# Performance work log

Measured on AMD Instinct MI355X. Metric: run time of the kernel, lower is better.

The kernel has to match this reference:

```python
import jax, jax.numpy as jnp
import numpy as np

KH, KW = 3, 3
PAD = 1
C_IN, C_OUT = 64, 128


def unfold(x, kh, kw, pad):
    # x: (B, C, H, W) -> (B, C, kh*kw, H*W), torch.nn.functional.unfold ordering
    B, C, H, W = x.shape
    xp = jnp.pad(x, ((0, 0), (0, 0), (pad, pad), (pad, pad)))
    patches = jnp.stack(
        [xp[:, :, i:i + H, j:j + W] for i in range(kh) for j in range(kw)],
        axis=2,
    )  # (B, C, K, H, W)
    return patches.reshape(B, C, kh * kw, H * W)


def setup_inputs() -> dict:
    key = jax.random.key(0)
    k1, k2, k3 = jax.random.split(key, 3)
    B, H, W = 8, 128, 128
    inp = jax.random.normal(k1, (B, C_IN, H, W), dtype=jnp.float32)
    g_buffer = jax.random.uniform(k2, (B, 2, H, W), dtype=jnp.float32)
    # weights param as in torch: (1, C*kh*kw, 1, out_channels), kaiming-uniform-ish
    wdepth = C_IN * KH * KW
    bound = float(np.sqrt(6.0 / wdepth))
    weights = jax.random.uniform(k3, (1, wdepth, 1, C_OUT), dtype=jnp.float32,
                                 minval=-bound, maxval=bound)
    bias = jnp.zeros((C_OUT,), dtype=jnp.float32)
    return {"input": inp, "g_buffer": g_buffer, "weights": weights, "bias": bias}


def reference(input, g_buffer, weights, bias):
    B, C, H, W = input.shape
    K = KH * KW
    L = H * W
    depth = 2.0 * (g_buffer[:, -1:, :, :] - 0.5)  # (B, 1, H, W)

    input_unf = unfold(input, KH, KW, PAD)          # (B, C, K, L)
    depth_unf = unfold(depth, KH, KW, PAD)          # (B, 1, K, L)

    # bilateral depth weighting
    dfeat = depth_unf - depth.reshape(B, 1, 1, L)   # (B, 1, K, L)
    dfeat = jnp.sum(dfeat * dfeat, axis=1)          # (B, K, L)
    wf = jnp.exp(-dfeat)
    wf = 9.0 * wf / jnp.sum(wf, axis=1, keepdims=True)  # (B, K, L)

    filt = input_unf * wf[:, None, :, :]            # (B, C, K, L)
    filt = filt.reshape(B, C * K, L)

    W2 = weights.reshape(C_OUT, C * K)              # raw reshape, matches torch .view
    out_unf = jnp.einsum('bkl,ok->bol', filt, W2)   # (B, C_OUT, L)
    out = out_unf.reshape(B, C_OUT, H, W) + bias[None, :, None, None]
    return out
```

## Files before the change

kernel.cpp:

```cpp
#include <hip/hip_runtime.h>
#include <hip/hip_bf16.h>
#include <stdint.h>

typedef _Float16 f16x8 __attribute__((ext_vector_type(8)));
typedef float    f32x4 __attribute__((ext_vector_type(4)));

#define CIN   64
#define COUT  128
#define HH    128
#define WW    128
#define BB    8

#define TROW  130
#define ROWBYTES (130 * 128)
#define TSIZE ((size_t)BB * TROW * ROWBYTES)

#define LROWB (34 * 128)
#define NCHKT (4 * 272)

#define AS1 __attribute__((address_space(1)))
#define AS3 __attribute__((address_space(3)))


__global__ void prep_plus(const float* __restrict__ wflat, _Float16* __restrict__ bp,
                          _Float16* __restrict__ T) {
    int gid = blockIdx.x * 256 + threadIdx.x;
    if (gid < 8 * 18 * 64 * 8) {
        int j = gid & 7;
        int l = (gid >> 3) & 63;
        int s = (gid >> 9) % 18;
        int n = gid / (18 * 512);
        int o = n * 16 + (l & 15);
        int c = ((s & 1) << 5) + ((l >> 4) << 3) + j;
        int k = s >> 1;
        bp[gid] = (_Float16)wflat[o * 576 + c * 9 + k];
        return;
    }
    int h = gid - 8 * 18 * 64 * 8;
    if (h < 16 * 1040) {
        int row = h / 1040, c = h - row * 1040;
        int b = row >> 1, yp = (row & 1) * 129;
        f16x8 z = {};
        *(f16x8*)((char*)T + (size_t)(b * TROW + yp) * ROWBYTES + c * 16) = z;
    }
}

__global__ __launch_bounds__(256) void transpose_pass(const float* __restrict__ inp,
                                                      _Float16* __restrict__ T) {
    __shared__ float sT[64][129];
    const int b   = blockIdx.x >> 7;
    const int y   = blockIdx.x & 127;
    const int tid = threadIdx.x;

    const float* ib = inp + ((long)b * CIN * HH + y) * WW;
    const int xq = tid & 31, c8 = tid >> 5;
    #pragma unroll
    for (int i = 0; i < 8; ++i) {
        int c = c8 * 8 + i;
        float4 v = *(const float4*)(ib + (long)c * (HH * WW) + (xq << 2));
        *(float4*)&sT[c][xq << 2] = v;
    }
    __syncthreads();

    const int x  = tid & 127;
    const int ch = tid >> 7;
    char* rowp = (char*)T + (size_t)(b * TROW + y + 1) * ROWBYTES + (size_t)(x + 1) * 128;
    const int sw = (x + 1) & 7;
    for (int c0 = ch * 8; c0 < 64; c0 += 16) {
        f16x8 v;
        #pragma unroll
        for (int j = 0; j < 8; ++j) v[j] = (_Float16)sT[c0 + j][x];
        *(f16x8*)(rowp + (((c0 >> 3) ^ sw) << 4)) = v;
    }
    if (tid < 16) {
        char* basep = (char*)T + (size_t)(b * TROW + y + 1) * ROWBYTES
                    + ((tid >> 3) ? 129 * 128 : 0) + (tid & 7) * 16;
        f16x8 z = {};
        *(f16x8*)basep = z;
    }
}

__global__ __launch_bounds__(256, 4) void depthcnn_main(
    const _Float16* __restrict__ T, const float* __restrict__ gbuf,
    const float* __restrict__ bias, const _Float16* __restrict__ aprep,
    float* __restrict__ out)
{
    __shared__ __align__(1024) char sIn[4 * LROWB];
    __shared__ _Float16 sWf[2][9][36];

    const int blk    = blockIdx.x;
    const int b      = blk & 7;
    const int rest   = blk >> 3;
    const int strip  = rest & 63;
    const int xq     = rest >> 6;
    const int ystart = strip << 1;
    const int x0     = xq << 5;

    const int tid  = threadIdx.x;
    const int wave = tid >> 6;
    const int lane = tid & 63;
    const int oi   = wave;
    const int l15  = lane & 15;
    const int g4   = lane >> 4;

    {
        const char* Tb = (const char*)T + ((size_t)b * TROW + ystart) * ROWBYTES
                       + (size_t)x0 * 128;
        #pragma unroll
        for (int tt = 0; tt < 5; ++tt) {
            int t = tt * 256 + tid;
            if (t < NCHKT) {
                int tr = t / 272, c = t - tr * 272;
                __builtin_amdgcn_global_load_lds(
                    (const AS1 uint32_t*)(Tb + (size_t)tr * ROWBYTES + c * 16),
                    (AS3 uint32_t*)(sIn + tr * LROWB + c * 16), 16, 0, 0);
            }
        }
    }

    const f16x8* __restrict__ ap = (const f16x8*)aprep;
    const char* wp0 = (const char*)ap + (size_t)((oi * 2 + 0) * 18) * 1024 + lane * 16;
    const char* wp1 = (const char*)ap + (size_t)((oi * 2 + 1) * 18) * 1024 + lane * 16;
    f16x8 af[2][2][2];
    af[0][0][0] = *(const f16x8*)(wp0);
    af[0][0][1] = *(const f16x8*)(wp0 + 1024);
    af[0][1][0] = *(const f16x8*)(wp1);
    af[0][1][1] = *(const f16x8*)(wp1 + 1024);

    if (tid < 64) {
        const int r = tid >> 5, pxl = tid & 31, x = x0 + pxl, y = ystart + r;
        const float* g = gbuf + ((size_t)b * 2 + 1) * (HH * WW);
        float dc = 2.f * (g[y * WW + x] - 0.5f);
        float e[9];
        float ssum = 0.f;
        #pragma unroll
        for (int k = 0; k < 9; ++k) {
            int yy = y + (k / 3) - 1;
            int xx = x + (k % 3) - 1;
            float dn = 0.f;
            if ((unsigned)yy < 128u && (unsigned)xx < 128u)
                dn = 2.f * (g[yy * WW + xx] - 0.5f);
            float df = dn - dc;
            float ek = __expf(-df * df);
            e[k] = ek;
            ssum += ek;
        }
        float sc = 9.f / ssum;
        #pragma unroll
        for (int k = 0; k < 9; ++k) sWf[r][k][pxl] = (_Float16)(e[k] * sc);
    }

    __syncthreads();

    const char* binA[3][2];
    #pragma unroll
    for (int d = 0; d < 3; ++d)
        #pragma unroll
        for (int ch = 0; ch < 2; ++ch)
            binA[d][ch] = sIn + (((l15 + d) << 7)
                        + ((((ch << 2) | g4) ^ ((l15 + d) & 7)) << 4));
    const char* bwf = (const char*)&sWf[0][0][0] + l15 * 2;

    f32x4 acc[2][2][2];
    #pragma unroll
    for (int r = 0; r < 2; ++r)
        #pragma unroll
        for (int t2 = 0; t2 < 2; ++t2)
            #pragma unroll
            for (int pt = 0; pt < 2; ++pt)
                acc[r][t2][pt] = (f32x4){0.f, 0.f, 0.f, 0.f};

    #pragma unroll
    for (int k = 0; k < 9; ++k) {
        if (k < 8) {
            const char* q0 = wp0 + (k + 1) * 2048;
            const char* q1 = wp1 + (k + 1) * 2048;
            af[(k + 1) & 1][0][0] = *(const f16x8*)(q0);
            af[(k + 1) & 1][0][1] = *(const f16x8*)(q0 + 1024);
            af[(k + 1) & 1][1][0] = *(const f16x8*)(q1);
            af[(k + 1) & 1][1][1] = *(const f16x8*)(q1 + 1024);
        }
        const int dy = k / 3;
        const int dx = k - 3 * dy;
        #pragma unroll
        for (int r = 0; r < 2; ++r) {
            _Float16 wh[2];
            #pragma unroll
            for (int pt = 0; pt < 2; ++pt)
                wh[pt] = *(const _Float16*)(bwf + ((r * 9 + k) * 72 + pt * 32));
            #pragma unroll
            for (int ch = 0; ch < 2; ++ch) {
                f16x8 bf[2];
                #pragma unroll
                for (int pt = 0; pt < 2; ++pt) {
                    f16x8 iv = *(const f16x8*)(binA[dx][ch]
                             + ((r + dy) * LROWB + (pt << 11)));
                    f16x8 w8 = {wh[pt], wh[pt], wh[pt], wh[pt],
                                wh[pt], wh[pt], wh[pt], wh[pt]};
                    bf[pt] = iv * w8;
                }
                #pragma unroll
                for (int t2 = 0; t2 < 2; ++t2)
                    #pragma unroll
                    for (int pt = 0; pt < 2; ++pt)
                        acc[r][t2][pt] = __builtin_amdgcn_mfma_f32_16x16x32_f16(
                            af[k & 1][t2][ch], bf[pt], acc[r][t2][pt], 0, 0, 0);
            }
        }
    }

    float* ob = out + (size_t)b * COUT * (HH * WW) + x0;
    #pragma unroll
    for (int r = 0; r < 2; ++r) {
        const int y = ystart + r;
        #pragma unroll
        for (int t2 = 0; t2 < 2; ++t2) {
            #pragma unroll
            for (int pt = 0; pt < 2; ++pt) {
                #pragma unroll
                for (int r4 = 0; r4 < 4; ++r4) {
                    const int o = (oi << 5) + (t2 << 4) + (g4 << 2) + r4;
                    ob[(size_t)o * (HH * WW) + (size_t)y * WW + (pt << 4) + l15]
                        = acc[r][t2][pt][r4] + bias[o];
                }
            }
        }
    }
}

extern "C" void kernel_launch(void* const* d_in, const int* in_sizes, int n_in,
                              void* d_out, int out_size, void* d_ws, size_t ws_size,
                              hipStream_t stream) {
    const float* inp  = (const float*)d_in[0];
    const float* gbuf = (const float*)d_in[1];
    const float* wts  = (const float*)d_in[2];
    const float* bias = (const float*)d_in[3];

    _Float16* T  = (_Float16*)d_ws;
    _Float16* bp = (_Float16*)((char*)d_ws + TSIZE);

    hipLaunchKernelGGL(prep_plus, dim3(353), dim3(256), 0, stream, wts, bp, T);
    hipLaunchKernelGGL(transpose_pass, dim3(BB * HH), dim3(256), 0, stream, inp, T);
    hipLaunchKernelGGL(depthcnn_main, dim3(2048), dim3(256), 0, stream,
                       T, gbuf, bias, bp, (float*)d_out);
}
```

Baseline: 49.60 us.

## Reorder taps dx-major to reuse LDS input rows across dy, spread depth-weight work

The tap loop now runs dx-outer and dy-inner. Each wave loads all four input rows for a given dx shift into registers once and reuses them for the three dy taps, which cuts repeated LDS reads. The weight prep kernel permutes its layout to match the new tap order. The bilateral weight computation is spread across all four waves instead of one. The transpose grid is reordered batch-minor and the occupancy hint drops from 4 to 3 to allow more registers, which costs some latency hiding.

New measurement: 49.25 us, median of 2. Within noise of the previous version (-0.7%).

```diff
diff --git a/kernel.cpp b/kernel.cpp
--- a/kernel.cpp
+++ b/kernel.cpp
@@ -26,13 +26,15 @@
                           _Float16* __restrict__ T) {
     int gid = blockIdx.x * 256 + threadIdx.x;
     if (gid < 8 * 18 * 64 * 8) {
-        int j = gid & 7;
-        int l = (gid >> 3) & 63;
-        int s = (gid >> 9) % 18;
-        int n = gid / (18 * 512);
-        int o = n * 16 + (l & 15);
-        int c = ((s & 1) << 5) + ((l >> 4) << 3) + j;
-        int k = s >> 1;
+        int j  = gid & 7;
+        int l  = (gid >> 3) & 63;
+        int sp = (gid >> 9) % 18;
+        int n  = gid / (18 * 512);
+        int o  = n * 16 + (l & 15);
+        int kp = sp >> 1;
+        int dx = kp / 3, dy = kp - 3 * dx;
+        int k  = dy * 3 + dx;
+        int c  = ((sp & 1) << 5) + ((l >> 4) << 3) + j;
         bp[gid] = (_Float16)wflat[o * 576 + c * 9 + k];
         return;
     }
@@ -48,8 +50,8 @@
 __global__ __launch_bounds__(256) void transpose_pass(const float* __restrict__ inp,
                                                       _Float16* __restrict__ T) {
     __shared__ float sT[64][129];
-    const int b   = blockIdx.x >> 7;
-    const int y   = blockIdx.x & 127;
+    const int b   = blockIdx.x & 7;
+    const int y   = blockIdx.x >> 3;
     const int tid = threadIdx.x;
 
     const float* ib = inp + ((long)b * CIN * HH + y) * WW;
@@ -80,7 +82,7 @@
     }
 }
 
-__global__ __launch_bounds__(256, 4) void depthcnn_main(
+__global__ __launch_bounds__(256, 3) void depthcnn_main(
     const _Float16* __restrict__ T, const float* __restrict__ gbuf,
     const float* __restrict__ bias, const _Float16* __restrict__ aprep,
     float* __restrict__ out)
@@ -127,8 +129,9 @@
     af[0][1][0] = *(const f16x8*)(wp1);
     af[0][1][1] = *(const f16x8*)(wp1 + 1024);
 
-    if (tid < 64) {
-        const int r = tid >> 5, pxl = tid & 31, x = x0 + pxl, y = ystart + r;
+    if (g4 == 0) {
+        const int item = (wave << 4) | l15;
+        const int r = item >> 5, pxl = item & 31, x = x0 + pxl, y = ystart + r;
         const float* g = gbuf + ((size_t)b * 2 + 1) * (HH * WW);
         float dc = 2.f * (g[y * WW + x] - 0.5f);
         float e[9];
@@ -152,6 +155,8 @@
 
     __syncthreads();
 
+    const char* bwf = (const char*)&sWf[0][0][0] + l15 * 2;
+
     const char* binA[3][2];
     #pragma unroll
     for (int d = 0; d < 3; ++d)
@@ -159,7 +164,6 @@
         for (int ch = 0; ch < 2; ++ch)
             binA[d][ch] = sIn + (((l15 + d) << 7)
                         + ((((ch << 2) | g4) ^ ((l15 + d) & 7)) << 4));
-    const char* bwf = (const char*)&sWf[0][0][0] + l15 * 2;
 
     f32x4 acc[2][2][2];
     #pragma unroll
@@ -171,40 +175,50 @@
                 acc[r][t2][pt] = (f32x4){0.f, 0.f, 0.f, 0.f};
 
     #pragma unroll
-    for (int k = 0; k < 9; ++k) {
-        if (k < 8) {
-            const char* q0 = wp0 + (k + 1) * 2048;
-            const char* q1 = wp1 + (k + 1) * 2048;
-            af[(k + 1) & 1][0][0] = *(const f16x8*)(q0);
-            af[(k + 1) & 1][0][1] = *(const f16x8*)(q0 + 1024);
-            af[(k + 1) & 1][1][0] = *(const f16x8*)(q1);
-            af[(k + 1) & 1][1][1] = *(const f16x8*)(q1 + 1024);
-        }
-        const int dy = k / 3;
-        const int dx = k - 3 * dy;
-        #pragma unroll
-        for (int r = 0; r < 2; ++r) {
-            _Float16 wh[2];
-            #pragma unroll
-            for (int pt = 0; pt < 2; ++pt)
-                wh[pt] = *(const _Float16*)(bwf + ((r * 9 + k) * 72 + pt * 32));
-            #pragma unroll
-            for (int ch = 0; ch < 2; ++ch) {
-                f16x8 bf[2];
-                #pragma unroll
-                for (int pt = 0; pt < 2; ++pt) {
-                    f16x8 iv = *(const f16x8*)(binA[dx][ch]
-                             + ((r + dy) * LROWB + (pt << 11)));
-                    f16x8 w8 = {wh[pt], wh[pt], wh[pt], wh[pt],
-                                wh[pt], wh[pt], wh[pt], wh[pt]};
-                    bf[pt] = iv * w8;
+    for (int dxi = 0; dxi < 3; ++dxi) {
+        f16x8 iv[4][2][2];
+        #pragma unroll
+        for (int t = 0; t < 4; ++t)
+            #pragma unroll
+            for (int ch = 0; ch < 2; ++ch)
+                #pragma unroll
+                for (int pt = 0; pt < 2; ++pt)
+                    iv[t][ch][pt] = *(const f16x8*)(binA[dxi][ch]
+                                  + (t * LROWB + (pt << 11)));
+        #pragma unroll
+        for (int dyi = 0; dyi < 3; ++dyi) {
+            const int kp = dxi * 3 + dyi;
+            const int k  = dyi * 3 + dxi;
+            if (kp < 8) {
+                const char* q0 = wp0 + (kp + 1) * 2048;
+                const char* q1 = wp1 + (kp + 1) * 2048;
+                af[(kp + 1) & 1][0][0] = *(const f16x8*)(q0);
+                af[(kp + 1) & 1][0][1] = *(const f16x8*)(q0 + 1024);
+                af[(kp + 1) & 1][1][0] = *(const f16x8*)(q1);
+                af[(kp + 1) & 1][1][1] = *(const f16x8*)(q1 + 1024);
+            }
+            #pragma unroll
+            for (int r = 0; r < 2; ++r) {
+                _Float16 wh[2];
+                #pragma unroll
+                for (int pt = 0; pt < 2; ++pt)
+                    wh[pt] = *(const _Float16*)(bwf + ((r * 9 + k) * 72 + pt * 32));
+                #pragma unroll
+                for (int ch = 0; ch < 2; ++ch) {
+                    f16x8 bf[2];
+                    #pragma unroll
+                    for (int pt = 0; pt < 2; ++pt) {
+                        f16x8 w8 = {wh[pt], wh[pt], wh[pt], wh[pt],
+                                    wh[pt], wh[pt], wh[pt], wh[pt]};
+                        bf[pt] = iv[r + dyi][ch][pt] * w8;
+                    }
+                    #pragma unroll
+                    for (int t2 = 0; t2 < 2; ++t2)
+                        #pragma unroll
+                        for (int pt = 0; pt < 2; ++pt)
+                            acc[r][t2][pt] = __builtin_amdgcn_mfma_f32_16x16x32_f16(
+                                af[kp & 1][t2][ch], bf[pt], acc[r][t2][pt], 0, 0, 0);
                 }
-                #pragma unroll
-                for (int t2 = 0; t2 < 2; ++t2)
-                    #pragma unroll
-                    for (int pt = 0; pt < 2; ++pt)
-                        acc[r][t2][pt] = __builtin_amdgcn_mfma_f32_16x16x32_f16(
-                            af[k & 1][t2][ch], bf[pt], acc[r][t2][pt], 0, 0, 0);
             }
         }
     }
```

## Process two tiles per block with double-buffered LDS prefetch of next tile

Applied to the files above, without the earlier changes.

The main kernel now runs 1024 persistent-ish blocks that each handle two tiles, staging the second tile's input rows and depth weights into a second LDS buffer while the first tile computes. The aim is to hide global-to-LDS load latency behind MFMA work and to amortise bias, offset and setup loads across tiles. The wait after the first tile uses a hand-picked vmcnt(16) that assumes how many global loads the compiler emits, which is fragile. LDS use doubles and occupancy may drop. The transpose kernel's block-to-(b,y) mapping is also reordered.

New measurement: 156.0 us. +214.5%, slower.

```diff
diff --git a/kernel.cpp b/kernel.cpp
--- a/kernel.cpp
+++ b/kernel.cpp
@@ -48,8 +48,8 @@
 __global__ __launch_bounds__(256) void transpose_pass(const float* __restrict__ inp,
                                                       _Float16* __restrict__ T) {
     __shared__ float sT[64][129];
-    const int b   = blockIdx.x >> 7;
-    const int y   = blockIdx.x & 127;
+    const int b   = blockIdx.x & 7;
+    const int y   = blockIdx.x >> 3;
     const int tid = threadIdx.x;
 
     const float* ib = inp + ((long)b * CIN * HH + y) * WW;
@@ -85,17 +85,10 @@
     const float* __restrict__ bias, const _Float16* __restrict__ aprep,
     float* __restrict__ out)
 {
-    __shared__ __align__(1024) char sIn[4 * LROWB];
-    __shared__ _Float16 sWf[2][9][36];
-
-    const int blk    = blockIdx.x;
-    const int b      = blk & 7;
-    const int rest   = blk >> 3;
-    const int strip  = rest & 63;
-    const int xq     = rest >> 6;
-    const int ystart = strip << 1;
-    const int x0     = xq << 5;
-
+    __shared__ __align__(1024) char sIn[2][4 * LROWB];
+    __shared__ _Float16 sWf[2][2][9][36];
+
+    const int p    = blockIdx.x;
     const int tid  = threadIdx.x;
     const int wave = tid >> 6;
     const int lane = tid & 63;
@@ -103,9 +96,31 @@
     const int l15  = lane & 15;
     const int g4   = lane >> 4;
 
-    {
-        const char* Tb = (const char*)T + ((size_t)b * TROW + ystart) * ROWBYTES
-                       + (size_t)x0 * 128;
+    const f16x8* __restrict__ ap = (const f16x8*)aprep;
+    const char* wp0 = (const char*)ap + (size_t)((oi * 2 + 0) * 18) * 1024 + lane * 16;
+    const char* wp1 = (const char*)ap + (size_t)((oi * 2 + 1) * 18) * 1024 + lane * 16;
+
+    float bv[2][4];
+    #pragma unroll
+    for (int t2 = 0; t2 < 2; ++t2)
+        #pragma unroll
+        for (int r4 = 0; r4 < 4; ++r4)
+            bv[t2][r4] = bias[(oi << 5) + (t2 << 4) + (g4 << 2) + r4];
+
+    int laneoff[3][2];
+    #pragma unroll
+    for (int d = 0; d < 3; ++d)
+        #pragma unroll
+        for (int ch = 0; ch < 2; ++ch)
+            laneoff[d][ch] = (((l15 + d) << 7)
+                           + ((((ch << 2) | g4) ^ ((l15 + d) & 7)) << 4));
+
+    auto stage = [&](int tile, int buf) {
+        const int b = tile & 7, rest = tile >> 3;
+        const int strip = rest & 63, xq = rest >> 6;
+        const char* Tb = (const char*)T + ((size_t)b * TROW + (strip << 1)) * ROWBYTES
+                       + (size_t)(xq << 5) * 128;
+        char* dst = &sIn[buf][0];
         #pragma unroll
         for (int tt = 0; tt < 5; ++tt) {
             int t = tt * 256 + tid;
@@ -113,117 +128,135 @@
                 int tr = t / 272, c = t - tr * 272;
                 __builtin_amdgcn_global_load_lds(
                     (const AS1 uint32_t*)(Tb + (size_t)tr * ROWBYTES + c * 16),
-                    (AS3 uint32_t*)(sIn + tr * LROWB + c * 16), 16, 0, 0);
-            }
-        }
-    }
-
-    const f16x8* __restrict__ ap = (const f16x8*)aprep;
-    const char* wp0 = (const char*)ap + (size_t)((oi * 2 + 0) * 18) * 1024 + lane * 16;
-    const char* wp1 = (const char*)ap + (size_t)((oi * 2 + 1) * 18) * 1024 + lane * 16;
-    f16x8 af[2][2][2];
-    af[0][0][0] = *(const f16x8*)(wp0);
-    af[0][0][1] = *(const f16x8*)(wp0 + 1024);
-    af[0][1][0] = *(const f16x8*)(wp1);
-    af[0][1][1] = *(const f16x8*)(wp1 + 1024);
-
-    if (tid < 64) {
-        const int r = tid >> 5, pxl = tid & 31, x = x0 + pxl, y = ystart + r;
-        const float* g = gbuf + ((size_t)b * 2 + 1) * (HH * WW);
-        float dc = 2.f * (g[y * WW + x] - 0.5f);
-        float e[9];
-        float ssum = 0.f;
+                    (AS3 uint32_t*)(dst + tr * LROWB + c * 16), 16, 0, 0);
+            }
+        }
+    };
+    auto wfcomp = [&](int tile, int buf) {
+        if (g4 == 0) {
+            const int b = tile & 7, rest = tile >> 3;
+            const int ystart = (rest & 63) << 1, x0 = (rest >> 6) << 5;
+            const int item = (wave << 4) | l15;
+            const int r = item >> 5, pxl = item & 31, x = x0 + pxl, y = ystart + r;
+            const float* g = gbuf + ((size_t)b * 2 + 1) * (HH * WW);
+            float dc = 2.f * (g[y * WW + x] - 0.5f);
+            float e[9];
+            float ssum = 0.f;
+            #pragma unroll
+            for (int k = 0; k < 9; ++k) {
+                int yy = y + (k / 3) - 1;
+                int xx = x + (k % 3) - 1;
+                float dn = 0.f;
+                if ((unsigned)yy < 128u && (unsigned)xx < 128u)
+                    dn = 2.f * (g[yy * WW + xx] - 0.5f);
+                float df = dn - dc;
+                float ek = __expf(-df * df);
+                e[k] = ek;
+                ssum += ek;
+            }
+            float sc = 9.f / ssum;
+            #pragma unroll
+            for (int k = 0; k < 9; ++k) sWf[buf][r][k][pxl] = (_Float16)(e[k] * sc);
+        }
+    };
+
+    stage(p, 0);
+    wfcomp(p, 0);
+    __syncthreads();
+
+    #pragma unroll 1
+    for (int i = 0; i < 2; ++i) {
+        const int tile = p + (i << 10);
+        const int buf  = i;
+
+        if (i == 0) {
+            stage(p + 1024, 1);
+            wfcomp(p + 1024, 1);
+        }
+
+        const char* sb  = &sIn[buf][0];
+        const char* bwf = (const char*)&sWf[buf][0][0][0] + l15 * 2;
+
+        f32x4 acc[2][2][2];
+        #pragma unroll
+        for (int r = 0; r < 2; ++r)
+            #pragma unroll
+            for (int t2 = 0; t2 < 2; ++t2)
+                #pragma unroll
+                for (int pt = 0; pt < 2; ++pt)
+                    acc[r][t2][pt] = (f32x4){0.f, 0.f, 0.f, 0.f};
+
+        f16x8 af[2][2][2];
+        af[0][0][0] = *(const f16x8*)(wp0);
+        af[0][0][1] = *(const f16x8*)(wp0 + 1024);
+        af[0][1][0] = *(const f16x8*)(wp1);
+        af[0][1][1] = *(const f16x8*)(wp1 + 1024);
+
         #pragma unroll
         for (int k = 0; k < 9; ++k) {
-            int yy = y + (k / 3) - 1;
-            int xx = x + (k % 3) - 1;
-            float dn = 0.f;
-            if ((unsigned)yy < 128u && (unsigned)xx < 128u)
-                dn = 2.f * (g[yy * WW + xx] - 0.5f);
-            float df = dn - dc;
-            float ek = __expf(-df * df);
-            e[k] = ek;
-            ssum += ek;
-        }
-        float sc = 9.f / ssum;
-        #pragma unroll
-        for (int k = 0; k < 9; ++k) sWf[r][k][pxl] = (_Float16)(e[k] * sc);
-    }
-
-    __syncthreads();
-
-    const char* binA[3][2];
-    #pragma unroll
-    for (int d = 0; d < 3; ++d)
-        #pragma unroll
-        for (int ch = 0; ch < 2; ++ch)
-            binA[d][ch] = sIn + (((l15 + d) << 7)
-                        + ((((ch << 2) | g4) ^ ((l15 + d) & 7)) << 4));
-    const char* bwf = (const char*)&sWf[0][0][0] + l15 * 2;
-
-    f32x4 acc[2][2][2];
-    #pragma unroll
-    for (int r = 0; r < 2; ++r)
-        #pragma unroll
-        for (int t2 = 0; t2 < 2; ++t2)
-            #pragma unroll
-            for (int pt = 0; pt < 2; ++pt)
-                acc[r][t2][pt] = (f32x4){0.f, 0.f, 0.f, 0.f};
-
-    #pragma unroll
-    for (int k = 0; k < 9; ++k) {
-        if (k < 8) {
-            const char* q0 = wp0 + (k + 1) * 2048;
-            const char* q1 = wp1 + (k + 1) * 2048;
-            af[(k + 1) & 1][0][0] = *(const f16x8*)(q0);
-            af[(k + 1) & 1][0][1] = *(const f16x8*)(q0 + 1024);
-            af[(k + 1) & 1][1][0] = *(const f16x8*)(q1);
-            af[(k + 1) & 1][1][1] = *(const f16x8*)(q1 + 1024);
-        }
-        const int dy = k / 3;
-        const int dx = k - 3 * dy;
-        #pragma unroll
-        for (int r = 0; r < 2; ++r) {
-            _Float16 wh[2];
-            #pragma unroll
-            for (int pt = 0; pt < 2; ++pt)
-                wh[pt] = *(const _Float16*)(bwf + ((r * 9 + k) * 72 + pt * 32));
-            #pragma unroll
-            for (int ch = 0; ch < 2; ++ch) {
-                f16x8 bf[2];
-                #pragma unroll
-                for (int pt = 0; pt < 2; ++pt) {
-                    f16x8 iv = *(const f16x8*)(binA[dx][ch]
-                             + ((r + dy) * LROWB + (pt << 11)));
-                    f16x8 w8 = {wh[pt], wh[pt], wh[pt], wh[pt],
-                                wh[pt], wh[pt], wh[pt], wh[pt]};
-                    bf[pt] = iv * w8;
+            if (k < 8) {
+                const char* q0 = wp0 + (k + 1) * 2048;
+                const char* q1 = wp1 + (k + 1) * 2048;
+                af[(k + 1) & 1][0][0] = *(const f16x8*)(q0);
+                af[(k + 1) & 1][0][1] = *(const f16x8*)(q0 + 1024);
+                af[(k + 1) & 1][1][0] = *(const f16x8*)(q1);
+                af[(k + 1) & 1][1][1] = *(const f16x8*)(q1 + 1024);
+            }
+            const int dy = k / 3;
+            const int dx = k - 3 * dy;
+            #pragma unroll
+            for (int r = 0; r < 2; ++r) {
+                _Float16 wh[2];
+                #pragma unroll
+                for (int pt = 0; pt < 2; ++pt)
+                    wh[pt] = *(const _Float16*)(bwf + ((r * 9 + k) * 72 + pt * 32));
+                #pragma unroll
+                for (int ch = 0; ch < 2; ++ch) {
+                    f16x8 bf[2];
+                    #pragma unroll
+                    for (int pt = 0; pt < 2; ++pt) {
+                        f16x8 iv = *(const f16x8*)(sb + laneoff[dx][ch]
+                                 + ((r + dy) * LROWB + (pt << 11)));
+                        f16x8 w8 = {wh[pt], wh[pt], wh[pt], wh[pt],
+                                    wh[pt], wh[pt], wh[pt], wh[pt]};
+                        bf[pt] = iv * w8;
+                    }
+                    #pragma unroll
+                    for (int t2 = 0; t2 < 2; ++t2)
+                        #pragma unroll
+                        for (int pt = 0; pt < 2; ++pt)
+                            acc[r][t2][pt] = __builtin_amdgcn_mfma_f32_16x16x32_f16(
+                                af[k & 1][t2][ch], bf[pt], acc[r][t2][pt], 0, 0, 0);
                 }
+            }
+        }
+
+        {
+            const int b = tile & 7, rest = tile >> 3;
+            const int ystart = (rest & 63) << 1, x0 = (rest >> 6) << 5;
+            float* ob = out + (size_t)b * COUT * (HH * WW) + x0;
+            #pragma unroll
+            for (int r = 0; r < 2; ++r) {
+                const int y = ystart + r;
                 #pragma unroll
                 for (int t2 = 0; t2 < 2; ++t2)
                     #pragma unroll
                     for (int pt = 0; pt < 2; ++pt)
-                        acc[r][t2][pt] = __builtin_amdgcn_mfma_f32_16x16x32_f16(
-                            af[k & 1][t2][ch], bf[pt], acc[r][t2][pt], 0, 0, 0);
-            }
-        }
-    }
-
-    float* ob = out + (size_t)b * COUT * (HH * WW) + x0;
-    #pragma unroll
-    for (int r = 0; r < 2; ++r) {
-        const int y = ystart + r;
-        #pragma unroll
-        for (int t2 = 0; t2 < 2; ++t2) {
-            #pragma unroll
-            for (int pt = 0; pt < 2; ++pt) {
-                #pragma unroll
-                for (int r4 = 0; r4 < 4; ++r4) {
-                    const int o = (oi << 5) + (t2 << 4) + (g4 << 2) + r4;
-                    ob[(size_t)o * (HH * WW) + (size_t)y * WW + (pt << 4) + l15]
-                        = acc[r][t2][pt][r4] + bias[o];
-                }
-            }
+                        #pragma unroll
+                        for (int r4 = 0; r4 < 4; ++r4) {
+                            const int o = (oi << 5) + (t2 << 4) + (g4 << 2) + r4;
+                            ob[(size_t)o * (HH * WW) + (size_t)y * WW + (pt << 4) + l15]
+                                = acc[r][t2][pt][r4] + bv[t2][r4];
+                        }
+            }
+        }
+
+        if (i == 0) {
+            __builtin_amdgcn_sched_barrier(0);
+            asm volatile("s_waitcnt vmcnt(16) lgkmcnt(0)" ::: "memory");
+            __builtin_amdgcn_sched_barrier(0);
+            __builtin_amdgcn_s_barrier();
+            __builtin_amdgcn_sched_barrier(0);
         }
     }
 }
@@ -241,6 +274,6 @@
 
     hipLaunchKernelGGL(prep_plus, dim3(353), dim3(256), 0, stream, wts, bp, T);
     hipLaunchKernelGGL(transpose_pass, dim3(BB * HH), dim3(256), 0, stream, inp, T);
-    hipLaunchKernelGGL(depthcnn_main, dim3(2048), dim3(256), 0, stream,
+    hipLaunchKernelGGL(depthcnn_main, dim3(1024), dim3(256), 0, stream,
                        T, gbuf, bias, bp, (float*)d_out);
 }
```
